# Performance work log

Measured on AMD Instinct MI355X. Metric: run time of the kernel, lower is better.

The kernel has to match this reference:

```python
import jax, jax.numpy as jnp
import numpy as np


def _patch_desc(x, patch_size):
    # x: (n, c, h, w). Replicate-pad by patch_size//2 and gather all
    # patch_size*patch_size shifted views -> (n, c*p*p, h*w) descriptors.
    n, c, h, w = x.shape
    step = patch_size // 2
    y = jnp.pad(x, ((0, 0), (0, 0), (step, step), (step, step)), mode='edge')
    feats = [y[:, :, i:i + h, j:j + w]
             for i in range(patch_size) for j in range(patch_size)]
    d = jnp.stack(feats, axis=2)            # (n, c, p*p, h, w)
    return d.reshape(n, c * patch_size * patch_size, h * w)


def setup_inputs() -> dict:
    key = jax.random.key(0)
    k1, k2 = jax.random.split(key)
    n, c, h, w = 4, 16, 64, 64
    s = jax.random.normal(k1, (n, c, h, w), dtype=jnp.float32)
    t = jax.random.normal(k2, (n, c, h, w), dtype=jnp.float32)
    return {"s": s, "t": t, "patch_size": 3}


def reference(s, t, patch_size):
    n, c, h, w = s.shape
    q = _patch_desc(s, patch_size)          # (n, d, hw) source queries
    p = _patch_desc(t, patch_size)          # (n, d, hw) target points
    # Squared-L2 nearest neighbor per source patch (exact version of FLANN kNN)
    qn = jnp.sum(q * q, axis=1)             # (n, hw)
    pn = jnp.sum(p * p, axis=1)             # (n, hw)
    cross = jnp.einsum('ndi,ndj->nij', q, p)  # (n, hw_q, hw_t)
    d2 = qn[:, :, None] - 2.0 * cross + pn[:, None, :]
    idx = jnp.argmin(d2, axis=2)            # (n, hw) flat target index
    nnd = jnp.min(d2, axis=2)               # (n, hw) squared distance
    idy = idx // w
    idx_x = idx % w
    nnf = jnp.stack([idy.reshape(n, h, w), idx_x.reshape(n, h, w)], axis=1)
    nnd = nnd.reshape(n, 1, h, w)
    return nnf.astype(jnp.int32), nnd
```

## Files before the change

kernel.cpp:

```cpp
#include <hip/hip_runtime.h>
#include <hip/hip_cooperative_groups.h>

namespace cg = cooperative_groups;


#define N_  4
#define C_  16
#define H_  64
#define W_  64
#define HW_ 4096
#define K_  160
#define SPLITS_M 4
#define KKSTRIDE 520

#define SPLITS_V 4
#define TILES_PER_SPLIT_V 4

typedef _Float16 f16;
typedef _Float16 f16x8 __attribute__((ext_vector_type(8)));
typedef float    f32x4 __attribute__((ext_vector_type(4)));

__device__ __forceinline__ int iclamp(int v, int lo, int hi) {
    return v < lo ? lo : (v > hi ? hi : v);
}

__device__ __forceinline__ void async_ld16(const void* g, void* l) {
    __builtin_amdgcn_global_load_lds(
        (const __attribute__((address_space(1))) unsigned int*)g,
        (__attribute__((address_space(3))) unsigned int*)l, 16, 0, 0);
}


__device__ __forceinline__
void desc_phase(char* smem, int y0, int n, int src, int tid,
                const float* __restrict__ s, const float* __restrict__ t,
                f16* __restrict__ Qh, f16* __restrict__ Ql,
                f16* __restrict__ Ph, f16* __restrict__ Pl,
                float* __restrict__ pn, float* __restrict__ qn) {
    float (*imgS)[C_][W_] = (float(*)[C_][W_])smem;
    float (*nS)[W_]       = (float(*)[W_])(smem + 12288);
    const float* img = (src ? s : t) + n * (C_ * HW_);
    f16* Dh = src ? Qh : Ph;
    f16* Dl = src ? Ql : Pl;
    float* nrm = src ? qn : pn;

    #pragma unroll
    for (int k = 0; k < 12; ++k) {
        const int idx = tid + k * 256;
        const int x = idx & 63, c = (idx >> 6) & 15, r = idx >> 10;
        const int gy = iclamp(y0 + r - 1, 0, H_ - 1);
        imgS[r][c][x] = img[c * HW_ + gy * W_ + x];
    }
    __syncthreads();

    const int q = tid >> 6, x = tid & 63;
    const int pix = y0 * W_ + x;
    float nacc = 0.f;
    #pragma unroll
    for (int u = 0; u < 5; ++u) {
        const int kk = q * 5 + u;
        f16x8 hv, lv;
        if (kk < 18) {
            const int d  = kk >> 1;
            const int c0 = (kk & 1) * 8;
            const int dy = (d * 11) >> 5;
            const int dx = d - dy * 3;
            const int xs = iclamp(x + dx - 1, 0, W_ - 1);
            #pragma unroll
            for (int cc = 0; cc < 8; ++cc) {
                const float v = imgS[dy][c0 + cc][xs];
                const f16 h = (f16)v;
                hv[cc] = h;
                lv[cc] = (f16)(v - (float)h);
                nacc += v * v;
            }
        } else {
            #pragma unroll
            for (int cc = 0; cc < 8; ++cc) { hv[cc] = (f16)0.f; lv[cc] = (f16)0.f; }
        }
        const size_t off = ((size_t)(n * 20 + kk) * HW_ + pix) * 8;
        *(f16x8*)&Dh[off] = hv;
        *(f16x8*)&Dl[off] = lv;
    }
    nS[q][x] = nacc;
    __syncthreads();
    if (tid < W_)
        nrm[n * HW_ + pix] = nS[0][tid] + nS[1][tid] + nS[2][tid] + nS[3][tid];
}

__device__ __forceinline__
void mfma_phase(char* smem, int split, int n, int iblk, int tid,
                const f16* __restrict__ Qh, const f16* __restrict__ Ql,
                const f16* __restrict__ Ph, const f16* __restrict__ Pl,
                const float* __restrict__ pn_g,
                unsigned long long* __restrict__ partial) {
    f16*   B0  = (f16*)smem;
    f16*   B1  = (f16*)(smem + 20 * KKSTRIDE * 2);
    float* pnS = (float*)(smem + 40 * KKSTRIDE * 2);

    const int wave = tid >> 6, lane = tid & 63;
    const int m = lane & 15, quad = lane >> 4;
    const int irow0 = iblk * 128 + wave * 32;

    f16x8 Ah[2][5], Al[2][5];
    #pragma unroll
    for (int is = 0; is < 2; ++is)
        #pragma unroll
        for (int kc = 0; kc < 5; ++kc) {
            const size_t off = ((size_t)(n * 20 + kc * 4 + quad) * HW_ +
                                irow0 + is * 16 + m) * 8;
            Ah[is][kc] = *(const f16x8*)(Qh + off);
            Al[is][kc] = *(const f16x8*)(Ql + off);
        }

    const int jsplit0 = split * 1024;
    #pragma unroll
    for (int k = 0; k < 4; ++k)
        pnS[tid + k * 256] = pn_g[n * HW_ + jsplit0 + tid + k * 256];

    float    bd[2][4];
    unsigned bj[2][4];
    #pragma unroll
    for (int is = 0; is < 2; ++is)
        #pragma unroll
        for (int rg = 0; rg < 4; ++rg) { bd[is][rg] = 3.0e38f; bj[is][rg] = 0u; }

    const int skk  = wave * 5;
    const int srow = lane & 31;
    const f16* sbase = (lane >> 5) ? Pl : Ph;

    #define STAGE(BUF, T)                                                     \
        {   _Pragma("unroll")                                                 \
            for (int u = 0; u < 5; ++u) {                                     \
                const int kk = skk + u;                                       \
                const f16* g = sbase + ((size_t)(n * 20 + kk) * HW_ +         \
                                        jsplit0 + (T) * 32 + srow) * 8;       \
                async_ld16(g, (void*)&BUF[kk * KKSTRIDE + lane * 8]);         \
            }                                                                 \
        }

    #define COMPUTE(BUF, T)                                                   \
        {   _Pragma("unroll")                                                 \
            for (int js = 0; js < 2; ++js) {                                  \
                f32x4 Cf[2];                                                  \
                Cf[0] = (f32x4){0.f, 0.f, 0.f, 0.f};                          \
                Cf[1] = (f32x4){0.f, 0.f, 0.f, 0.f};                          \
                _Pragma("unroll")                                             \
                for (int kc = 0; kc < 5; ++kc) {                              \
                    const int kb = (kc * 4 + quad) * KKSTRIDE +               \
                                   (js * 16 + m) * 8;                         \
                    const f16x8 bh = *(const f16x8*)&BUF[kb];                 \
                    const f16x8 bl = *(const f16x8*)&BUF[kb + 256];           \
                    _Pragma("unroll")                                         \
                    for (int is = 0; is < 2; ++is) {                          \
                        Cf[is] = __builtin_amdgcn_mfma_f32_16x16x32_f16(      \
                            Ah[is][kc], bh, Cf[is], 0, 0, 0);                 \
                        Cf[is] = __builtin_amdgcn_mfma_f32_16x16x32_f16(      \
                            Al[is][kc], bh, Cf[is], 0, 0, 0);                 \
                        Cf[is] = __builtin_amdgcn_mfma_f32_16x16x32_f16(      \
                            Ah[is][kc], bl, Cf[is], 0, 0, 0);                 \
                    }                                                         \
                }                                                             \
                const int jloc = (T) * 32 + js * 16 + m;                      \
                const float pnv = pnS[jloc];                                  \
                _Pragma("unroll")                                             \
                for (int is = 0; is < 2; ++is)                                \
                    _Pragma("unroll")                                         \
                    for (int rg = 0; rg < 4; ++rg) {                          \
                        const float d = fmaf(Cf[is][rg], -2.f, pnv);          \
                        if (d < bd[is][rg]) {       \
                            bd[is][rg] = d;                                   \
                            bj[is][rg] = (unsigned)jloc;                      \
                        }                                                     \
                    }                                                         \
            }                                                                 \
        }

    STAGE(B0, 0)
    asm volatile("s_waitcnt vmcnt(0)" ::: "memory");
    __syncthreads();

    for (int jt = 0; jt < 32; jt += 2) {
        if (jt + 1 < 32) STAGE(B1, jt + 1)
        COMPUTE(B0, jt)
        asm volatile("s_waitcnt vmcnt(0)" ::: "memory");
        __syncthreads();
        if (jt + 2 < 32) STAGE(B0, jt + 2)
        COMPUTE(B1, jt + 1)
        asm volatile("s_waitcnt vmcnt(0)" ::: "memory");
        __syncthreads();
    }
    #undef STAGE
    #undef COMPUTE

    #pragma unroll
    for (int is = 0; is < 2; ++is)
        #pragma unroll
        for (int rg = 0; rg < 4; ++rg) {
            float    d = bd[is][rg];
            unsigned j = (unsigned)jsplit0 + bj[is][rg];
            #pragma unroll
            for (int off = 1; off < 16; off <<= 1) {
                const float    od = __shfl_xor(d, off, 64);
                const unsigned oj = __shfl_xor(j, off, 64);
                const bool take = (od < d) || (od == d && oj < j);
                d = take ? od : d;
                j = take ? oj : j;
            }
            if (m == 0) {
                const int i = irow0 + is * 16 + quad * 4 + rg;
                partial[(size_t)(split * N_ + n) * HW_ + i] =
                    ((unsigned long long)j << 32) |
                    (unsigned long long)__float_as_uint(d);
            }
        }
}

__device__ __forceinline__
void finalize_phase(int id, const unsigned long long* __restrict__ partial,
                    const float* __restrict__ qn_g, float* __restrict__ out) {
    const int n   = id >> 12;
    const int pix = id & 4095;
    float    bd = 3.0e38f;
    unsigned bj = 0u;
    #pragma unroll
    for (int sp = 0; sp < SPLITS_M; ++sp) {
        const unsigned long long v = partial[(size_t)(sp * N_ + n) * HW_ + pix];
        const float    d = __uint_as_float((unsigned)(v & 0xffffffffull));
        const unsigned j = (unsigned)(v >> 32);
        const bool take = (d < bd) || (d == bd && j < bj);
        bd = take ? d : bd;
        bj = take ? j : bj;
    }
    out[n * 2 * HW_ + pix]            = (float)(bj >> 6);
    out[n * 2 * HW_ + HW_ + pix]      = (float)(bj & 63);
    out[N_ * 2 * HW_ + n * HW_ + pix] = bd + qn_g[n * HW_ + pix];
}

__global__ __launch_bounds__(256)
void fused_nn_kernel(const float* __restrict__ s, const float* __restrict__ t,
                     f16* __restrict__ Qh, f16* __restrict__ Ql,
                     f16* __restrict__ Ph, f16* __restrict__ Pl,
                     float* __restrict__ pn, float* __restrict__ qn,
                     unsigned long long* __restrict__ partial,
                     float* __restrict__ out) {
    __shared__ __align__(16) char smem[45696];
    const int bid = blockIdx.x;
    const int tid = threadIdx.x;
    cg::grid_group grid = cg::this_grid();

    desc_phase(smem, bid & 63, (bid >> 6) & 3, bid >> 8, tid,
               s, t, Qh, Ql, Ph, Pl, pn, qn);
    __threadfence();
    grid.sync();

    mfma_phase(smem, bid & 3, (bid >> 2) & 3, bid >> 4, tid,
               Qh, Ql, Ph, Pl, pn, partial);
    __threadfence();
    grid.sync();

    if (bid < 64) finalize_phase(bid * 256 + tid, partial, qn, out);
}

__global__ __launch_bounds__(256)
void build_desc_norms_kernel(const float* __restrict__ s,
                             const float* __restrict__ t,
                             f16* __restrict__ Qh, f16* __restrict__ Ql,
                             f16* __restrict__ Ph, f16* __restrict__ Pl,
                             float* __restrict__ pn,
                             float* __restrict__ qn) {
    __shared__ __align__(16) char smem[13312];
    desc_phase(smem, blockIdx.x, blockIdx.y, blockIdx.z, threadIdx.x,
               s, t, Qh, Ql, Ph, Pl, pn, qn);
}

__global__ __launch_bounds__(256)
void mfma_nn_kernel(const f16* __restrict__ Qh, const f16* __restrict__ Ql,
                    const f16* __restrict__ Ph, const f16* __restrict__ Pl,
                    const float* __restrict__ pn_g,
                    unsigned long long* __restrict__ partial) {
    __shared__ __align__(16) char smem[45696];
    const int bid = blockIdx.x;
    mfma_phase(smem, bid & 3, (bid >> 2) & 3, bid >> 4, threadIdx.x,
               Qh, Ql, Ph, Pl, pn_g, partial);
}

__global__ __launch_bounds__(256)
void finalize_mfma_kernel(const unsigned long long* __restrict__ partial,
                          const float* __restrict__ qn_g,
                          float* __restrict__ out) {
    finalize_phase(blockIdx.x * 256 + threadIdx.x, partial, qn_g, out);
}

__global__ __launch_bounds__(256)
void patchmatch_mono_kernel(const float* __restrict__ s,
                            const float* __restrict__ t,
                            float* __restrict__ out) {
    const int yq  = blockIdx.x;
    const int n   = blockIdx.y;
    const int tid = threadIdx.x;
    const int tx  = tid & 15;
    const int ty  = tid >> 4;
    const int i0  = ty * 4;
    const int jrow = tx >> 3;
    const int jx0  = (tx & 7) * 8;

    __shared__ float qS[C_][3][68];
    __shared__ float tS[C_][4][68];
    __shared__ float pnS[HW_];
    __shared__ float qnS[W_];

    const float* sb = s + n * (C_ * HW_);
    const float* tb = t + n * (C_ * HW_);

    for (int jj = tid; jj < HW_; jj += 256) {
        const int y = jj >> 6, x = jj & 63;
        float acc = 0.f;
        for (int c = 0; c < C_; ++c) {
            const float* tc = tb + c * HW_;
            #pragma unroll
            for (int dy = 0; dy < 3; ++dy) {
                const float* tr = tc + iclamp(y + dy - 1, 0, H_ - 1) * W_;
                #pragma unroll
                for (int dx = 0; dx < 3; ++dx) {
                    float v = tr[iclamp(x + dx - 1, 0, W_ - 1)];
                    acc += v * v;
                }
            }
        }
        pnS[jj] = acc;
    }
    for (int idx = tid; idx < C_ * 3 * 66; idx += 256) {
        const int c   = idx / (3 * 66);
        const int rem = idx - c * (3 * 66);
        const int rr  = rem / 66;
        const int xi  = rem - rr * 66;
        qS[c][rr][xi] = sb[c * HW_ + iclamp(yq + rr - 1, 0, H_ - 1) * W_ +
                           iclamp(xi - 1, 0, W_ - 1)];
    }
    __syncthreads();
    if (tid < W_) {
        float acc = 0.f;
        for (int c = 0; c < C_; ++c)
            #pragma unroll
            for (int dy = 0; dy < 3; ++dy)
                #pragma unroll
                for (int dx = 0; dx < 3; ++dx) {
                    float v = qS[c][dy][tid + dx];
                    acc += v * v;
                }
        qnS[tid] = acc;
    }

    unsigned long long best[4] = {~0ull, ~0ull, ~0ull, ~0ull};
    for (int yt = 0; yt < 32; ++yt) {
        __syncthreads();
        for (int idx = tid; idx < C_ * 4 * 66; idx += 256) {
            const int c   = idx / (4 * 66);
            const int rem = idx - c * (4 * 66);
            const int rr  = rem / 66;
            const int xi  = rem - rr * 66;
            tS[c][rr][xi] = tb[c * HW_ + iclamp(2 * yt + rr - 1, 0, H_ - 1) * W_ +
                               iclamp(xi - 1, 0, W_ - 1)];
        }
        __syncthreads();

        float acc[4][8];
        #pragma unroll
        for (int a = 0; a < 4; ++a)
            #pragma unroll
            for (int b = 0; b < 8; ++b) acc[a][b] = 0.f;

        for (int c = 0; c < C_; ++c) {
            #pragma unroll
            for (int dy = 0; dy < 3; ++dy) {
                float qv[8], tv[12];
                *(float4*)&qv[0] = *(const float4*)&qS[c][dy][i0];
                *(float4*)&qv[4] = *(const float4*)&qS[c][dy][i0 + 4];
                const float* trow = &tS[c][jrow + dy][jx0];
                *(float4*)&tv[0] = *(const float4*)&trow[0];
                *(float4*)&tv[4] = *(const float4*)&trow[4];
                *(float4*)&tv[8] = *(const float4*)&trow[8];
                #pragma unroll
                for (int dx = 0; dx < 3; ++dx)
                    #pragma unroll
                    for (int a = 0; a < 4; ++a)
                        #pragma unroll
                        for (int b = 0; b < 8; ++b)
                            acc[a][b] += qv[a + dx] * tv[b + dx];
            }
        }
        const int rbase = (2 * yt + jrow) * W_ + jx0;
        #pragma unroll
        for (int a = 0; a < 4; ++a) {
            const float qn = qnS[i0 + a];
            #pragma unroll
            for (int b = 0; b < 8; ++b) {
                const int j = rbase + b;
                const float d2 = qn + pnS[j] - 2.f * acc[a][b];
                unsigned long long cand =
                    ((unsigned long long)__float_as_uint(d2) << 32) | (unsigned)j;
                best[a] = cand < best[a] ? cand : best[a];
            }
        }
    }
    #pragma unroll
    for (int a = 0; a < 4; ++a) {
        unsigned long long v = best[a];
        #pragma unroll
        for (int mm = 8; mm >= 1; mm >>= 1) {
            unsigned long long o = __shfl_xor(v, mm, 64);
            v = o < v ? o : v;
        }
        best[a] = v;
    }
    if (tx == 0) {
        #pragma unroll
        for (int a = 0; a < 4; ++a) {
            const int x = i0 + a;
            const unsigned j = (unsigned)(best[a] & 0xffffffffu);
            const float d2 = __uint_as_float((unsigned)(best[a] >> 32));
            const int pix = yq * W_ + x;
            out[n * 2 * HW_ + pix]            = (float)(j >> 6);
            out[n * 2 * HW_ + HW_ + pix]      = (float)(j & 63);
            out[N_ * 2 * HW_ + n * HW_ + pix] = d2;
        }
    }
}

extern "C" void kernel_launch(void* const* d_in, const int* in_sizes, int n_in,
                              void* d_out, int out_size, void* d_ws, size_t ws_size,
                              hipStream_t stream) {
    const float* s = (const float*)d_in[0];
    const float* t = (const float*)d_in[1];
    float* out = (float*)d_out;

    const size_t norm_b  = (size_t)N_ * HW_ * 4;
    const size_t part_b  = (size_t)SPLITS_M * N_ * HW_ * 8;
    const size_t desc_b  = (size_t)N_ * HW_ * K_ * 2;
    const size_t need_m  = 2 * norm_b + part_b + 4 * desc_b;

    if (ws_size >= need_m) {
        char* w = (char*)d_ws;
        float* pn = (float*)w;                       w += norm_b;
        float* qn = (float*)w;                       w += norm_b;
        unsigned long long* partial = (unsigned long long*)w; w += part_b;
        f16* Qh = (f16*)w;  w += desc_b;
        f16* Ql = (f16*)w;  w += desc_b;
        f16* Ph = (f16*)w;  w += desc_b;
        f16* Pl = (f16*)w;

        int dev = 0;
        (void)hipGetDevice(&dev);
        int coop = 0;
        (void)hipDeviceGetAttribute(&coop, hipDeviceAttributeCooperativeLaunch,
                                    dev);
        int nCU = 0;
        (void)hipDeviceGetAttribute(&nCU, hipDeviceAttributeMultiprocessorCount,
                                    dev);
        int maxBlk = 0;
        (void)hipOccupancyMaxActiveBlocksPerMultiprocessor(
            &maxBlk, (const void*)fused_nn_kernel, 256, 0);

        if (coop && (long long)maxBlk * nCU >= 512) {
            void* args[] = { (void*)&s, (void*)&t, (void*)&Qh, (void*)&Ql,
                             (void*)&Ph, (void*)&Pl, (void*)&pn, (void*)&qn,
                             (void*)&partial, (void*)&out };
            hipError_t err = hipLaunchCooperativeKernel(
                (const void*)fused_nn_kernel, dim3(512), dim3(256), args, 0,
                stream);
            if (err == hipSuccess) return;
        }

        build_desc_norms_kernel<<<dim3(64, N_, 2), 256, 0, stream>>>(
            s, t, Qh, Ql, Ph, Pl, pn, qn);
        mfma_nn_kernel<<<512, 256, 0, stream>>>(Qh, Ql, Ph, Pl, pn, partial);
        finalize_mfma_kernel<<<64, 256, 0, stream>>>(partial, qn, out);
        return;
    }

    dim3 grid(H_, N_);
    patchmatch_mono_kernel<<<grid, 256, 0, stream>>>(s, t, out);
}
```

Measured before the change: 126.0 us.

## Replace cooperative grid-sync kernel with two launches and last-block finalize

Drops the cooperative fused kernel and its per-call device attribute and occupancy queries. Descriptor building stays a separate kernel, which also zeroes a per-row-block counter array. The mfma kernel now does the cross-split argmin reduction in whichever block finishes last, detected with an atomic counter, which removes both grid-wide barriers and the separate finalize launch. The trade-off is a kernel launch boundary in place of one grid barrier, plus an atomic and fence per block.

```diff
diff --git a/kernel.cpp b/kernel.cpp
--- a/kernel.cpp
+++ b/kernel.cpp
@@ -1,7 +1,4 @@
 #include <hip/hip_runtime.h>
-#include <hip/hip_cooperative_groups.h>
-
-namespace cg = cooperative_groups;
 
 
 #define N_  4
@@ -13,9 +10,6 @@
 #define SPLITS_M 4
 #define KKSTRIDE 520
 
-#define SPLITS_V 4
-#define TILES_PER_SPLIT_V 4
-
 typedef _Float16 f16;
 typedef _Float16 f16x8 __attribute__((ext_vector_type(8)));
 typedef float    f32x4 __attribute__((ext_vector_type(4)));
@@ -30,20 +24,29 @@
         (__attribute__((address_space(3))) unsigned int*)l, 16, 0, 0);
 }
 
-
-__device__ __forceinline__
-void desc_phase(char* smem, int y0, int n, int src, int tid,
-                const float* __restrict__ s, const float* __restrict__ t,
-                f16* __restrict__ Qh, f16* __restrict__ Ql,
-                f16* __restrict__ Ph, f16* __restrict__ Pl,
-                float* __restrict__ pn, float* __restrict__ qn) {
-    float (*imgS)[C_][W_] = (float(*)[C_][W_])smem;
-    float (*nS)[W_]       = (float(*)[W_])(smem + 12288);
+__global__ __launch_bounds__(256)
+void build_desc_norms_kernel(const float* __restrict__ s,
+                             const float* __restrict__ t,
+                             f16* __restrict__ Qh, f16* __restrict__ Ql,
+                             f16* __restrict__ Ph, f16* __restrict__ Pl,
+                             float* __restrict__ pn,
+                             float* __restrict__ qn,
+                             unsigned* __restrict__ done) {
+    const int y0  = blockIdx.x;
+    const int n   = blockIdx.y;
+    const int src = blockIdx.z;
+    const int tid = threadIdx.x;
+
+    if (y0 == 0 && n == 0 && src == 0 && tid < N_ * 32)
+        done[tid] = 0u;
+
     const float* img = (src ? s : t) + n * (C_ * HW_);
     f16* Dh = src ? Qh : Ph;
     f16* Dl = src ? Ql : Pl;
     float* nrm = src ? qn : pn;
 
+    __shared__ float imgS[3][C_][W_];
+    __shared__ float nS[4][W_];
     #pragma unroll
     for (int k = 0; k < 12; ++k) {
         const int idx = tid + k * 256;
@@ -88,19 +91,27 @@
         nrm[n * HW_ + pix] = nS[0][tid] + nS[1][tid] + nS[2][tid] + nS[3][tid];
 }
 
-__device__ __forceinline__
-void mfma_phase(char* smem, int split, int n, int iblk, int tid,
-                const f16* __restrict__ Qh, const f16* __restrict__ Ql,
-                const f16* __restrict__ Ph, const f16* __restrict__ Pl,
-                const float* __restrict__ pn_g,
-                unsigned long long* __restrict__ partial) {
-    f16*   B0  = (f16*)smem;
-    f16*   B1  = (f16*)(smem + 20 * KKSTRIDE * 2);
-    float* pnS = (float*)(smem + 40 * KKSTRIDE * 2);
-
+__global__ __launch_bounds__(256)
+void mfma_nn_kernel(const f16* __restrict__ Qh, const f16* __restrict__ Ql,
+                    const f16* __restrict__ Ph, const f16* __restrict__ Pl,
+                    const float* __restrict__ pn_g,
+                    const float* __restrict__ qn_g,
+                    unsigned long long* __restrict__ partial,
+                    unsigned* __restrict__ done,
+                    float* __restrict__ out) {
+    const int bid   = blockIdx.x;
+    const int split = bid & 3;
+    const int n     = (bid >> 2) & 3;
+    const int iblk  = bid >> 4;
+    const int tid  = threadIdx.x;
     const int wave = tid >> 6, lane = tid & 63;
     const int m = lane & 15, quad = lane >> 4;
     const int irow0 = iblk * 128 + wave * 32;
+
+    __shared__ f16 B0[20 * KKSTRIDE];
+    __shared__ f16 B1[20 * KKSTRIDE];
+    __shared__ float pnS[1024];
+    __shared__ int lastS;
 
     f16x8 Ah[2][5], Al[2][5];
     #pragma unroll
@@ -214,82 +225,34 @@
                     (unsigned long long)__float_as_uint(d);
             }
         }
-}
-
-__device__ __forceinline__
-void finalize_phase(int id, const unsigned long long* __restrict__ partial,
-                    const float* __restrict__ qn_g, float* __restrict__ out) {
-    const int n   = id >> 12;
-    const int pix = id & 4095;
-    float    bd = 3.0e38f;
-    unsigned bj = 0u;
-    #pragma unroll
-    for (int sp = 0; sp < SPLITS_M; ++sp) {
-        const unsigned long long v = partial[(size_t)(sp * N_ + n) * HW_ + pix];
-        const float    d = __uint_as_float((unsigned)(v & 0xffffffffull));
-        const unsigned j = (unsigned)(v >> 32);
-        const bool take = (d < bd) || (d == bd && j < bj);
-        bd = take ? d : bd;
-        bj = take ? j : bj;
-    }
-    out[n * 2 * HW_ + pix]            = (float)(bj >> 6);
-    out[n * 2 * HW_ + HW_ + pix]      = (float)(bj & 63);
-    out[N_ * 2 * HW_ + n * HW_ + pix] = bd + qn_g[n * HW_ + pix];
-}
-
-__global__ __launch_bounds__(256)
-void fused_nn_kernel(const float* __restrict__ s, const float* __restrict__ t,
-                     f16* __restrict__ Qh, f16* __restrict__ Ql,
-                     f16* __restrict__ Ph, f16* __restrict__ Pl,
-                     float* __restrict__ pn, float* __restrict__ qn,
-                     unsigned long long* __restrict__ partial,
-                     float* __restrict__ out) {
-    __shared__ __align__(16) char smem[45696];
-    const int bid = blockIdx.x;
-    const int tid = threadIdx.x;
-    cg::grid_group grid = cg::this_grid();
-
-    desc_phase(smem, bid & 63, (bid >> 6) & 3, bid >> 8, tid,
-               s, t, Qh, Ql, Ph, Pl, pn, qn);
+
     __threadfence();
-    grid.sync();
-
-    mfma_phase(smem, bid & 3, (bid >> 2) & 3, bid >> 4, tid,
-               Qh, Ql, Ph, Pl, pn, partial);
-    __threadfence();
-    grid.sync();
-
-    if (bid < 64) finalize_phase(bid * 256 + tid, partial, qn, out);
-}
-
-__global__ __launch_bounds__(256)
-void build_desc_norms_kernel(const float* __restrict__ s,
-                             const float* __restrict__ t,
-                             f16* __restrict__ Qh, f16* __restrict__ Ql,
-                             f16* __restrict__ Ph, f16* __restrict__ Pl,
-                             float* __restrict__ pn,
-                             float* __restrict__ qn) {
-    __shared__ __align__(16) char smem[13312];
-    desc_phase(smem, blockIdx.x, blockIdx.y, blockIdx.z, threadIdx.x,
-               s, t, Qh, Ql, Ph, Pl, pn, qn);
-}
-
-__global__ __launch_bounds__(256)
-void mfma_nn_kernel(const f16* __restrict__ Qh, const f16* __restrict__ Ql,
-                    const f16* __restrict__ Ph, const f16* __restrict__ Pl,
-                    const float* __restrict__ pn_g,
-                    unsigned long long* __restrict__ partial) {
-    __shared__ __align__(16) char smem[45696];
-    const int bid = blockIdx.x;
-    mfma_phase(smem, bid & 3, (bid >> 2) & 3, bid >> 4, threadIdx.x,
-               Qh, Ql, Ph, Pl, pn_g, partial);
-}
-
-__global__ __launch_bounds__(256)
-void finalize_mfma_kernel(const unsigned long long* __restrict__ partial,
-                          const float* __restrict__ qn_g,
-                          float* __restrict__ out) {
-    finalize_phase(blockIdx.x * 256 + threadIdx.x, partial, qn_g, out);
+    __syncthreads();
+    if (tid == 0)
+        lastS = (atomicAdd(&done[n * 32 + iblk], 1u) == 3u) ? 1 : 0;
+    __syncthreads();
+    if (lastS) {
+        __threadfence();
+        if (tid < 128) {
+            const int pix = iblk * 128 + tid;
+            float    fbd = 3.0e38f;
+            unsigned fbj = 0u;
+            #pragma unroll
+            for (int sp = 0; sp < SPLITS_M; ++sp) {
+                const unsigned long long v =
+                    partial[(size_t)(sp * N_ + n) * HW_ + pix];
+                const float    d = __uint_as_float((unsigned)(v & 0xffffffffull));
+                const unsigned j = (unsigned)(v >> 32);
+                const bool take = (d < fbd) || (d == fbd && j < fbj);
+                fbd = take ? d : fbd;
+                fbj = take ? j : fbj;
+            }
+            out[n * 2 * HW_ + pix]       = (float)(fbj >> 6);
+            out[n * 2 * HW_ + HW_ + pix] = (float)(fbj & 63);
+            out[N_ * 2 * HW_ + n * HW_ + pix] =
+                fbd + qn_g[n * HW_ + pix];
+        }
+    }
 }
 
 __global__ __launch_bounds__(256)
@@ -437,45 +400,25 @@
 
     const size_t norm_b  = (size_t)N_ * HW_ * 4;
     const size_t part_b  = (size_t)SPLITS_M * N_ * HW_ * 8;
+    const size_t done_b  = 512;
     const size_t desc_b  = (size_t)N_ * HW_ * K_ * 2;
-    const size_t need_m  = 2 * norm_b + part_b + 4 * desc_b;
+    const size_t need_m  = 2 * norm_b + part_b + done_b + 4 * desc_b;
 
     if (ws_size >= need_m) {
         char* w = (char*)d_ws;
         float* pn = (float*)w;                       w += norm_b;
         float* qn = (float*)w;                       w += norm_b;
         unsigned long long* partial = (unsigned long long*)w; w += part_b;
+        unsigned* done = (unsigned*)w;               w += done_b;
         f16* Qh = (f16*)w;  w += desc_b;
         f16* Ql = (f16*)w;  w += desc_b;
         f16* Ph = (f16*)w;  w += desc_b;
         f16* Pl = (f16*)w;
 
-        int dev = 0;
-        (void)hipGetDevice(&dev);
-        int coop = 0;
-        (void)hipDeviceGetAttribute(&coop, hipDeviceAttributeCooperativeLaunch,
-                                    dev);
-        int nCU = 0;
-        (void)hipDeviceGetAttribute(&nCU, hipDeviceAttributeMultiprocessorCount,
-                                    dev);
-        int maxBlk = 0;
-        (void)hipOccupancyMaxActiveBlocksPerMultiprocessor(
-            &maxBlk, (const void*)fused_nn_kernel, 256, 0);
-
-        if (coop && (long long)maxBlk * nCU >= 512) {
-            void* args[] = { (void*)&s, (void*)&t, (void*)&Qh, (void*)&Ql,
-                             (void*)&Ph, (void*)&Pl, (void*)&pn, (void*)&qn,
-                             (void*)&partial, (void*)&out };
-            hipError_t err = hipLaunchCooperativeKernel(
-                (const void*)fused_nn_kernel, dim3(512), dim3(256), args, 0,
-                stream);
-            if (err == hipSuccess) return;
-        }
-
         build_desc_norms_kernel<<<dim3(64, N_, 2), 256, 0, stream>>>(
-            s, t, Qh, Ql, Ph, Pl, pn, qn);
-        mfma_nn_kernel<<<512, 256, 0, stream>>>(Qh, Ql, Ph, Pl, pn, partial);
-        finalize_mfma_kernel<<<64, 256, 0, stream>>>(partial, qn, out);
+            s, t, Qh, Ql, Ph, Pl, pn, qn, done);
+        mfma_nn_kernel<<<512, 256, 0, stream>>>(
+            Qh, Ql, Ph, Pl, pn, qn, partial, done, out);
         return;
     }
 
```

Measured after the change: 177.4 us. 40.7% more time.
